# Optimization experiments

Hardware: AMD Instinct MI355X
Metric: run time of the kernel (lower is better)

## Reference

```python
import jax, jax.numpy as jnp
import numpy as np

NUM_EMBEDDINGS = 2048
EMBEDDING_DIM = 256
COMMITMENT_COST = 0.25


def setup_inputs() -> dict:
    key = jax.random.key(0)
    k1, k2 = jax.random.split(key)
    inputs = jax.random.normal(k1, (2, EMBEDDING_DIM, 24, 24, 24), dtype=jnp.float32)
    embedding_weight = jax.random.normal(k2, (NUM_EMBEDDINGS, EMBEDDING_DIM), dtype=jnp.float32)
    return {"inputs": inputs, "embedding_weight": embedding_weight}


def reference(inputs, embedding_weight):
    # [B, C, D, H, W] -> [B, D, H, W, C]
    x = jnp.transpose(inputs, (0, 2, 3, 4, 1))
    in_shape = x.shape
    flat = x.reshape(-1, EMBEDDING_DIM)  # [N, D]

    distances = (
        jnp.sum(flat * flat, axis=1, keepdims=True)
        + jnp.sum(embedding_weight * embedding_weight, axis=1)
        - 2.0 * flat @ embedding_weight.T
    )
    encoding_indices = jnp.argmin(distances, axis=1)  # [N]
    encodings = jax.nn.one_hot(encoding_indices, NUM_EMBEDDINGS, dtype=jnp.float32)  # [N, K]

    # Gather instead of one_hot @ W (same math, no redundant GEMM)
    quantized = embedding_weight[encoding_indices].reshape(in_shape)

    e_latent_loss = jnp.mean((jax.lax.stop_gradient(quantized) - x) ** 2)
    loss = COMMITMENT_COST * e_latent_loss

    # Straight-through estimator
    quantized_st = x + jax.lax.stop_gradient(quantized - x)

    avg_probs = jnp.mean(encodings, axis=0)
    perplexity = jnp.exp(-jnp.sum(avg_probs * jnp.log(avg_probs + 1e-10)))

    quantized_out = jnp.transpose(quantized_st, (0, 4, 1, 2, 3))
    return (loss, quantized_out, perplexity, encodings, encoding_indices[:, None])
```

## Files before the change

### kernel.cpp

```cpp
#include <hip/hip_runtime.h>

#define S_SP   13824
#define CHAN   256
#define NQ     27648
#define KCODES 2048
#define CS     3538944
#define OFF_Q   1
#define OFF_PPL 7077889
#define OFF_ENC 7077890LL
#define OFF_IDX 63700994LL

typedef __bf16 bf16x8 __attribute__((ext_vector_type(8)));
typedef float  f32x4  __attribute__((ext_vector_type(4)));

#define GLOAD_LDS16(g, s)                                                      \
  __builtin_amdgcn_global_load_lds(                                            \
      (const __attribute__((address_space(1))) void*)(g),                      \
      (__attribute__((address_space(3))) void*)(s), 16, 0, 0)

__device__ __forceinline__ unsigned int f2bf(float f) {
  unsigned int u = __float_as_uint(f);
  unsigned int r = u + 0x7FFFu + ((u >> 16) & 1u);
  return r >> 16;
}
__device__ __forceinline__ float bf2f(unsigned int h) {
  return __uint_as_float(h << 16);
}
__device__ __forceinline__ void fsplit(float f, unsigned int& hi, unsigned int& lo) {
  hi = f2bf(f);
  float r = f - bf2f(hi);
  lo = f2bf(r);
}

__global__ __launch_bounds__(256) void prep_wx(const float* __restrict__ W,
                                               const float* __restrict__ X,
                                               unsigned short* __restrict__ Wh,
                                               unsigned short* __restrict__ Wl,
                                               float* __restrict__ wn,
                                               unsigned short* __restrict__ Xh,
                                               unsigned short* __restrict__ Xl,
                                               float* __restrict__ xn,
                                               int* __restrict__ zero_base) {
  __shared__ float xs[32 * 257];
  int t = threadIdx.x;
  if (blockIdx.x < 256) {
    if (blockIdx.x == 0) {
      for (int j = t; j < 2050; j += 256) zero_base[j] = 0;
    }
    int g = blockIdx.x * 256 + t;
    int row = g >> 5;
    int d0 = (g & 31) * 8;
    const float* Wp = W + (size_t)row * CHAN + d0;
    float v[8];
    *(float4*)(v) = *(const float4*)Wp;
    *(float4*)(v + 4) = *(const float4*)(Wp + 4);
    float s = 0.f;
    unsigned int h[8], l[8];
#pragma unroll
    for (int j = 0; j < 8; ++j) {
      s = fmaf(v[j], v[j], s);
      fsplit(v[j], h[j], l[j]);
    }
    int4 ph, pl;
    ph.x = (int)(h[0] | (h[1] << 16)); ph.y = (int)(h[2] | (h[3] << 16));
    ph.z = (int)(h[4] | (h[5] << 16)); ph.w = (int)(h[6] | (h[7] << 16));
    pl.x = (int)(l[0] | (l[1] << 16)); pl.y = (int)(l[2] | (l[3] << 16));
    pl.z = (int)(l[4] | (l[5] << 16)); pl.w = (int)(l[6] | (l[7] << 16));
    *(int4*)(Wh + (size_t)row * CHAN + d0) = ph;
    *(int4*)(Wl + (size_t)row * CHAN + d0) = pl;
    for (int off = 16; off; off >>= 1) s += __shfl_down(s, off);
    if ((t & 31) == 0) wn[row] = s;
    return;
  }
  int qb = (blockIdx.x - 256) * 32;
  int b = qb / S_SP, s0 = qb % S_SP;
  const float* xp = X + (size_t)b * CS + s0;
  int q = t & 31;
  int db = t >> 5;
  for (int r = 0; r < 32; ++r) {
    int d = db + (r << 3);
    xs[q * 257 + d] = xp[(size_t)d * S_SP + q];
  }
  __syncthreads();
  int row = t >> 3, c8 = t & 7;
  size_t obase = (size_t)(qb + row) * CHAN;
  const float* rp0 = xs + row * 257;
  float ss = 0.f;
#pragma unroll
  for (int j = 0; j < 4; ++j) {
    int d = j * 64 + c8 * 8;
    const float* rp = rp0 + d;
    unsigned int h[8], l[8];
#pragma unroll
    for (int e = 0; e < 8; ++e) {
      float v = rp[e];
      ss = fmaf(v, v, ss);
      fsplit(v, h[e], l[e]);
    }
    int4 ph, pl;
    ph.x = (int)(h[0] | (h[1] << 16)); ph.y = (int)(h[2] | (h[3] << 16));
    ph.z = (int)(h[4] | (h[5] << 16)); ph.w = (int)(h[6] | (h[7] << 16));
    pl.x = (int)(l[0] | (l[1] << 16)); pl.y = (int)(l[2] | (l[3] << 16));
    pl.z = (int)(l[4] | (l[5] << 16)); pl.w = (int)(l[6] | (l[7] << 16));
    *(int4*)(Xh + obase + d) = ph;
    *(int4*)(Xl + obase + d) = pl;
  }
  ss += __shfl_xor(ss, 1);
  ss += __shfl_xor(ss, 2);
  ss += __shfl_xor(ss, 4);
  if (c8 == 0) xn[qb + row] = ss;
}

__global__ __launch_bounds__(256, 2) void dist_mfma(const unsigned short* __restrict__ Xh,
                                                    const unsigned short* __restrict__ Xl,
                                                    const unsigned short* __restrict__ Wh,
                                                    const unsigned short* __restrict__ Wl,
                                                    const float* __restrict__ wn,
                                                    float* __restrict__ rB1,
                                                    int* __restrict__ rI1,
                                                    float* __restrict__ rB2) {
  __shared__ __align__(16) unsigned short sW[2][2][4096];
  __shared__ float wnl[1024];
  int t = threadIdx.x;
  int w = t >> 6, l = t & 63;
  int lr = l & 15, lc = l >> 4;
  int kg = blockIdx.x & 1;
  int qb = (blockIdx.x >> 1) * 128;
  int kofs = kg << 10;

  for (int j = t; j < 1024; j += 256) wnl[j] = wn[kofs + j];

  bf16x8 ah[2][8], al[2][8];
#pragma unroll
  for (int s = 0; s < 2; ++s) {
    size_t base = (size_t)(qb + w * 32 + s * 16 + lr) * CHAN + lc * 8;
#pragma unroll
    for (int c = 0; c < 8; ++c) {
      ah[s][c] = *(const bf16x8*)(Xh + base + c * 32);
      al[s][c] = *(const bf16x8*)(Xl + base + c * 32);
    }
  }

  float b1[2][4], b2[2][4]; int i1[2][4];
#pragma unroll
  for (int s = 0; s < 2; ++s)
#pragma unroll
    for (int r = 0; r < 4; ++r) { b1[s][r] = 3.4e38f; b2[s][r] = 3.4e38f; i1[s][r] = 0; }

  auto stage = [&](int buf, int kt) {
    size_t rb = (size_t)(kofs + (kt << 4) + lr) * CHAN + lc * 8;
    GLOAD_LDS16(Wh + rb + w * 32,        &sW[buf][0][w * 512]);
    GLOAD_LDS16(Wh + rb + (w + 4) * 32,  &sW[buf][0][(w + 4) * 512]);
    GLOAD_LDS16(Wl + rb + w * 32,        &sW[buf][1][w * 512]);
    GLOAD_LDS16(Wl + rb + (w + 4) * 32,  &sW[buf][1][(w + 4) * 512]);
  };

  stage(0, 0);
  __syncthreads();

  for (int kt = 0; kt < 64; ++kt) {
    int cur = kt & 1;
    if (kt < 63) stage(cur ^ 1, kt + 1);
    f32x4 a0 = {0.f, 0.f, 0.f, 0.f}, a1 = {0.f, 0.f, 0.f, 0.f};
#pragma unroll
    for (int c = 0; c < 8; ++c) {
      bf16x8 bh = *(const bf16x8*)&sW[cur][0][c * 512 + (l << 3)];
      bf16x8 bl = *(const bf16x8*)&sW[cur][1][c * 512 + (l << 3)];
      a0 = __builtin_amdgcn_mfma_f32_16x16x32_bf16(ah[0][c], bh, a0, 0, 0, 0);
      a1 = __builtin_amdgcn_mfma_f32_16x16x32_bf16(ah[1][c], bh, a1, 0, 0, 0);
      a0 = __builtin_amdgcn_mfma_f32_16x16x32_bf16(al[0][c], bh, a0, 0, 0, 0);
      a1 = __builtin_amdgcn_mfma_f32_16x16x32_bf16(al[1][c], bh, a1, 0, 0, 0);
      a0 = __builtin_amdgcn_mfma_f32_16x16x32_bf16(ah[0][c], bl, a0, 0, 0, 0);
      a1 = __builtin_amdgcn_mfma_f32_16x16x32_bf16(ah[1][c], bl, a1, 0, 0, 0);
    }
    int k = kofs + (kt << 4) + lr;
    float wnk = wnl[(kt << 4) + lr];
#pragma unroll
    for (int r = 0; r < 4; ++r) {
      float s0 = fmaf(-2.0f, a0[r], wnk);
      bool lt0 = s0 < b1[0][r];
      b2[0][r] = fminf(b2[0][r], fmaxf(s0, b1[0][r]));
      b1[0][r] = lt0 ? s0 : b1[0][r];
      i1[0][r] = lt0 ? k : i1[0][r];
      float s1 = fmaf(-2.0f, a1[r], wnk);
      bool lt1 = s1 < b1[1][r];
      b2[1][r] = fminf(b2[1][r], fmaxf(s1, b1[1][r]));
      b1[1][r] = lt1 ? s1 : b1[1][r];
      i1[1][r] = lt1 ? k : i1[1][r];
    }
    __syncthreads();
  }

#pragma unroll
  for (int m = 1; m < 16; m <<= 1) {
#pragma unroll
    for (int s = 0; s < 2; ++s)
#pragma unroll
      for (int r = 0; r < 4; ++r) {
        float ob1 = __shfl_xor(b1[s][r], m);
        int   oi  = __shfl_xor(i1[s][r], m);
        float ob2 = __shfl_xor(b2[s][r], m);
        bool sw = (ob1 < b1[s][r]) || (ob1 == b1[s][r] && oi < i1[s][r]);
        b2[s][r] = fminf(fmaxf(b1[s][r], ob1), fminf(b2[s][r], ob2));
        b1[s][r] = sw ? ob1 : b1[s][r];
        i1[s][r] = sw ? oi : i1[s][r];
      }
  }
  if (lr == 0) {
#pragma unroll
    for (int s = 0; s < 2; ++s)
#pragma unroll
      for (int r = 0; r < 4; ++r) {
        int q = qb + w * 32 + s * 16 + lc * 4 + r;
        size_t o = (size_t)kg * NQ + q;
        rB1[o] = b1[s][r]; rI1[o] = i1[s][r]; rB2[o] = b2[s][r];
      }
  }
}

__global__ __launch_bounds__(256) void merge_k(const float* __restrict__ rB1,
                                               const int* __restrict__ rI1,
                                               const float* __restrict__ rB2,
                                               const float* __restrict__ xn,
                                               float* __restrict__ idx_out,
                                               int* __restrict__ flagcount,
                                               int2* __restrict__ flaglist,
                                               int* __restrict__ counts,
                                               float* __restrict__ loss_acc) {
  __shared__ float wred[4];
  int t = threadIdx.x;
  int n = blockIdx.x * 256 + t;
  float B1 = rB1[n]; int I1 = rI1[n]; float B2 = rB2[n];
  float c1 = rB1[NQ + n]; int ci = rI1[NQ + n]; float c2 = rB2[NQ + n];
  bool sw = (c1 < B1) || (c1 == B1 && ci < I1);
  float nb2 = fminf(fmaxf(B1, c1), fminf(B2, c2));
  float nb1 = sw ? c1 : B1;
  int   ni  = sw ? ci : I1;
  if (nb2 - nb1 < 0.05f) {
    int slot = atomicAdd(flagcount, 1);
    flaglist[slot] = make_int2(n, ni);
  }
  idx_out[n] = (float)ni;
  atomicAdd(&counts[ni], 1);

  float lq = xn[n] + nb1;
  for (int off = 32; off; off >>= 1) lq += __shfl_down(lq, off);
  if ((t & 63) == 0) wred[t >> 6] = lq;
  __syncthreads();
  if (t == 0) atomicAdd(loss_acc, wred[0] + wred[1] + wred[2] + wred[3]);
}

__global__ __launch_bounds__(256) void refine2(const float* __restrict__ X,
                                               const float* __restrict__ W,
                                               const int* __restrict__ flagcount,
                                               const int2* __restrict__ flaglist,
                                               float* __restrict__ idx_out,
                                               int* __restrict__ counts) {
  __shared__ double xd[CHAN];
  __shared__ double rv[256];
  __shared__ int    ri[256];
  int t = threadIdx.x;
  int cnt = flagcount[0];
  for (int jj = blockIdx.x; jj < cnt; jj += gridDim.x) {
    __syncthreads();
    int2 e = flaglist[jj];
    int n = e.x, prov = e.y;
    int b = n / S_SP, s = n % S_SP;
    xd[t] = (double)X[(size_t)b * CS + (size_t)t * S_SP + s];
    __syncthreads();

    double best = 1e300;
    int bi = 1 << 30;
    for (int j8 = 0; j8 < 8; ++j8) {
      int k = t * 8 + j8;
      const float* Wp = W + (size_t)k * CHAN;
      double dsum = 0.0;
      for (int d = 0; d < CHAN; ++d) {
        double df = xd[d] - (double)Wp[d];
        dsum = fma(df, df, dsum);
      }
      if (dsum < best) { best = dsum; bi = k; }
    }
    rv[t] = best; ri[t] = bi;
    __syncthreads();
    for (int off = 128; off > 0; off >>= 1) {
      if (t < off) {
        if (rv[t + off] < rv[t] || (rv[t + off] == rv[t] && ri[t + off] < ri[t])) {
          rv[t] = rv[t + off]; ri[t] = ri[t + off];
        }
      }
      __syncthreads();
    }
    if (t == 0) {
      int fin = ri[0];
      idx_out[n] = (float)fin;
      if (fin != prov) {
        atomicAdd(&counts[prov], -1);
        atomicAdd(&counts[fin], 1);
      }
    }
  }
}

__global__ __launch_bounds__(256) void emit_q(const float* __restrict__ W,
                                              float* __restrict__ outF) {
  __shared__ int sidx[64];
  int t = threadIdx.x;
  int qb = blockIdx.x * 64;
  if (t < 64) sidx[t] = (int)outF[OFF_IDX + qb + t];
  __syncthreads();

  {
    f32x4 z = {0.f, 0.f, 0.f, 0.f};
    float* rp = outF + OFF_ENC + (size_t)qb * KCODES + t * 4;
#pragma unroll 4
    for (int q = 0; q < 64; ++q) {
      *(f32x4*)rp = z;
      *(f32x4*)(rp + 1024) = z;
      rp += KCODES;
    }
  }
  __syncthreads();
  if (t < 64) outF[OFF_ENC + (size_t)(qb + t) * KCODES + sidx[t]] = 1.0f;

  int q = t & 63, cg = t >> 6;
  int n = qb + q;
  int idx = sidx[q];
  int b = n / S_SP, s = n % S_SP;
  const float* Wp = W + (size_t)idx * CHAN;
  float* qp = outF + OFF_Q + (size_t)b * CS + s;
#pragma unroll 8
  for (int k = 0; k < 64; ++k) {
    int c = cg + (k << 2);
    qp[(size_t)c * S_SP] = Wp[c];
  }
}

__global__ __launch_bounds__(256) void finalize(const int* __restrict__ counts,
                                                const float* __restrict__ loss_acc,
                                                float* __restrict__ outF) {
  __shared__ double red[256];
  int t = threadIdx.x;
  double H = 0.0;
  for (int k = t; k < KCODES; k += 256) {
    double p = (double)counts[k] / (double)NQ;
    H += p * log(p + 1e-10);
  }
  red[t] = H;
  __syncthreads();
  for (int off = 128; off > 0; off >>= 1) {
    if (t < off) red[t] += red[t + off];
    __syncthreads();
  }
  if (t == 0) {
    outF[0] = 0.25f * (loss_acc[0] / 7077888.0f);
    outF[OFF_PPL] = (float)exp(-red[0]);
  }
}

extern "C" void kernel_launch(void* const* d_in, const int* in_sizes, int n_in,
                              void* d_out, int out_size, void* d_ws, size_t ws_size,
                              hipStream_t stream) {
  const float* X = (const float*)d_in[0];
  const float* W = (const float*)d_in[1];
  float* outF = (float*)d_out;
  char* ws = (char*)d_ws;
  float* wn        = (float*)ws;
  int*   counts    = (int*)(ws + 8192);
  float* loss_acc  = (float*)(ws + 16384);
  int*   flagcount = (int*)(ws + 16388);
  int2*  flaglist  = (int2*)(ws + 32768);
  float* rB1       = (float*)(ws + 262144);
  int*   rI1       = (int*)(ws + 483328);
  float* rB2       = (float*)(ws + 704512);
  float* xn        = (float*)(ws + 925696);
  unsigned short* Wh = (unsigned short*)(ws + 1048576);
  unsigned short* Wl = (unsigned short*)(ws + 2097152);
  unsigned short* Xh = (unsigned short*)(ws + 3145728);
  unsigned short* Xl = Xh + (size_t)NQ * CHAN;

  prep_wx<<<256 + NQ / 32, 256, 0, stream>>>(W, X, Wh, Wl, wn, Xh, Xl, xn,
                                             (int*)(ws + 8192));
  dist_mfma<<<(NQ / 128) * 2, 256, 0, stream>>>(Xh, Xl, Wh, Wl, wn, rB1, rI1, rB2);
  merge_k<<<NQ / 256, 256, 0, stream>>>(rB1, rI1, rB2, xn, outF + OFF_IDX,
                                        flagcount, flaglist, counts, loss_acc);
  refine2<<<256, 256, 0, stream>>>(X, W, flagcount, flaglist, outF + OFF_IDX, counts);
  emit_q<<<NQ / 64, 256, 0, stream>>>(W, outF);
  finalize<<<1, 256, 0, stream>>>(counts, loss_acc, outF);
}
```

Measured before the change: 261.5 us.

## Stream codebook tiles into registers directly, dropping LDS staging and barriers

```diff
diff --git a/kernel.cpp b/kernel.cpp
--- a/kernel.cpp
+++ b/kernel.cpp
@@ -12,11 +12,6 @@
 
 typedef __bf16 bf16x8 __attribute__((ext_vector_type(8)));
 typedef float  f32x4  __attribute__((ext_vector_type(4)));
-
-#define GLOAD_LDS16(g, s)                                                      \
-  __builtin_amdgcn_global_load_lds(                                            \
-      (const __attribute__((address_space(1))) void*)(g),                      \
-      (__attribute__((address_space(3))) void*)(s), 16, 0, 0)
 
 __device__ __forceinline__ unsigned int f2bf(float f) {
   unsigned int u = __float_as_uint(f);
@@ -119,7 +114,6 @@
                                                     float* __restrict__ rB1,
                                                     int* __restrict__ rI1,
                                                     float* __restrict__ rB2) {
-  __shared__ __align__(16) unsigned short sW[2][2][4096];
   __shared__ float wnl[1024];
   int t = threadIdx.x;
   int w = t >> 6, l = t & 63;
@@ -147,34 +141,7 @@
 #pragma unroll
     for (int r = 0; r < 4; ++r) { b1[s][r] = 3.4e38f; b2[s][r] = 3.4e38f; i1[s][r] = 0; }
 
-  auto stage = [&](int buf, int kt) {
-    size_t rb = (size_t)(kofs + (kt << 4) + lr) * CHAN + lc * 8;
-    GLOAD_LDS16(Wh + rb + w * 32,        &sW[buf][0][w * 512]);
-    GLOAD_LDS16(Wh + rb + (w + 4) * 32,  &sW[buf][0][(w + 4) * 512]);
-    GLOAD_LDS16(Wl + rb + w * 32,        &sW[buf][1][w * 512]);
-    GLOAD_LDS16(Wl + rb + (w + 4) * 32,  &sW[buf][1][(w + 4) * 512]);
-  };
-
-  stage(0, 0);
-  __syncthreads();
-
-  for (int kt = 0; kt < 64; ++kt) {
-    int cur = kt & 1;
-    if (kt < 63) stage(cur ^ 1, kt + 1);
-    f32x4 a0 = {0.f, 0.f, 0.f, 0.f}, a1 = {0.f, 0.f, 0.f, 0.f};
-#pragma unroll
-    for (int c = 0; c < 8; ++c) {
-      bf16x8 bh = *(const bf16x8*)&sW[cur][0][c * 512 + (l << 3)];
-      bf16x8 bl = *(const bf16x8*)&sW[cur][1][c * 512 + (l << 3)];
-      a0 = __builtin_amdgcn_mfma_f32_16x16x32_bf16(ah[0][c], bh, a0, 0, 0, 0);
-      a1 = __builtin_amdgcn_mfma_f32_16x16x32_bf16(ah[1][c], bh, a1, 0, 0, 0);
-      a0 = __builtin_amdgcn_mfma_f32_16x16x32_bf16(al[0][c], bh, a0, 0, 0, 0);
-      a1 = __builtin_amdgcn_mfma_f32_16x16x32_bf16(al[1][c], bh, a1, 0, 0, 0);
-      a0 = __builtin_amdgcn_mfma_f32_16x16x32_bf16(ah[0][c], bl, a0, 0, 0, 0);
-      a1 = __builtin_amdgcn_mfma_f32_16x16x32_bf16(ah[1][c], bl, a1, 0, 0, 0);
-    }
-    int k = kofs + (kt << 4) + lr;
-    float wnk = wnl[(kt << 4) + lr];
+  auto select = [&](const f32x4& a0, const f32x4& a1, int k, float wnk) {
 #pragma unroll
     for (int r = 0; r < 4; ++r) {
       float s0 = fmaf(-2.0f, a0[r], wnk);
@@ -188,8 +155,51 @@
       b1[1][r] = lt1 ? s1 : b1[1][r];
       i1[1][r] = lt1 ? k : i1[1][r];
     }
-    __syncthreads();
-  }
+  };
+
+  __syncthreads();
+
+  const unsigned short* ph  = Wh + (size_t)(kofs + lr) * CHAN + lc * 8;
+  const unsigned short* pl_ = Wl + (size_t)(kofs + lr) * CHAN + lc * 8;
+
+  bf16x8 bh[4], bl[4];
+#pragma unroll
+  for (int c = 0; c < 4; ++c) {
+    bh[c] = *(const bf16x8*)(ph + c * 32);
+    bl[c] = *(const bf16x8*)(pl_ + c * 32);
+  }
+
+  f32x4 pa0, pa1;
+  int   pk = 0;
+  float pwnk = 0.f;
+
+  for (int kt = 0; kt < 64; ++kt) {
+    f32x4 a0 = {0.f, 0.f, 0.f, 0.f}, a1 = {0.f, 0.f, 0.f, 0.f};
+#pragma unroll
+    for (int c = 0; c < 8; ++c) {
+      const int sl = c & 3;
+      a0 = __builtin_amdgcn_mfma_f32_16x16x32_bf16(ah[0][c], bh[sl], a0, 0, 0, 0);
+      a1 = __builtin_amdgcn_mfma_f32_16x16x32_bf16(ah[1][c], bh[sl], a1, 0, 0, 0);
+      a0 = __builtin_amdgcn_mfma_f32_16x16x32_bf16(al[0][c], bh[sl], a0, 0, 0, 0);
+      a1 = __builtin_amdgcn_mfma_f32_16x16x32_bf16(al[1][c], bh[sl], a1, 0, 0, 0);
+      a0 = __builtin_amdgcn_mfma_f32_16x16x32_bf16(ah[0][c], bl[sl], a0, 0, 0, 0);
+      a1 = __builtin_amdgcn_mfma_f32_16x16x32_bf16(ah[1][c], bl[sl], a1, 0, 0, 0);
+      if (c < 4) {
+        bh[sl] = *(const bf16x8*)(ph + (c + 4) * 32);
+        bl[sl] = *(const bf16x8*)(pl_ + (c + 4) * 32);
+      } else {
+        bh[sl] = *(const bf16x8*)(ph + 16 * CHAN + (c - 4) * 32);
+        bl[sl] = *(const bf16x8*)(pl_ + 16 * CHAN + (c - 4) * 32);
+      }
+    }
+    if (kt) select(pa0, pa1, pk, pwnk);
+    pa0 = a0; pa1 = a1;
+    pk = kofs + (kt << 4) + lr;
+    pwnk = wnl[(kt << 4) + lr];
+    ph  += 16 * CHAN;
+    pl_ += 16 * CHAN;
+  }
+  select(pa0, pa1, pk, pwnk);
 
 #pragma unroll
   for (int m = 1; m < 16; m <<= 1) {
```

After: 398.2 us. +52.3%, slower.

## Switch distance GEMM to 32x32x16 MFMA with software-pipelined argmin selection

Applied to the files above, without the earlier changes.

```diff
diff --git a/kernel.cpp b/kernel.cpp
--- a/kernel.cpp
+++ b/kernel.cpp
@@ -12,6 +12,7 @@
 
 typedef __bf16 bf16x8 __attribute__((ext_vector_type(8)));
 typedef float  f32x4  __attribute__((ext_vector_type(4)));
+typedef float  f32x16 __attribute__((ext_vector_type(16)));
 
 #define GLOAD_LDS16(g, s)                                                      \
   __builtin_amdgcn_global_load_lds(                                            \
@@ -119,102 +120,110 @@
                                                     float* __restrict__ rB1,
                                                     int* __restrict__ rI1,
                                                     float* __restrict__ rB2) {
-  __shared__ __align__(16) unsigned short sW[2][2][4096];
+  __shared__ __align__(16) unsigned short sW[2][2][8192];
   __shared__ float wnl[1024];
   int t = threadIdx.x;
   int w = t >> 6, l = t & 63;
-  int lr = l & 15, lc = l >> 4;
+  int lcol = l & 31;
+  int lkg  = l >> 5;
   int kg = blockIdx.x & 1;
   int qb = (blockIdx.x >> 1) * 128;
   int kofs = kg << 10;
 
   for (int j = t; j < 1024; j += 256) wnl[j] = wn[kofs + j];
 
-  bf16x8 ah[2][8], al[2][8];
-#pragma unroll
-  for (int s = 0; s < 2; ++s) {
-    size_t base = (size_t)(qb + w * 32 + s * 16 + lr) * CHAN + lc * 8;
-#pragma unroll
-    for (int c = 0; c < 8; ++c) {
-      ah[s][c] = *(const bf16x8*)(Xh + base + c * 32);
-      al[s][c] = *(const bf16x8*)(Xl + base + c * 32);
-    }
-  }
-
-  float b1[2][4], b2[2][4]; int i1[2][4];
-#pragma unroll
-  for (int s = 0; s < 2; ++s)
-#pragma unroll
-    for (int r = 0; r < 4; ++r) { b1[s][r] = 3.4e38f; b2[s][r] = 3.4e38f; i1[s][r] = 0; }
+  bf16x8 ah[16], al[16];
+  {
+    size_t base = (size_t)(qb + w * 32 + lcol) * CHAN + (lkg << 3);
+#pragma unroll
+    for (int kc = 0; kc < 16; ++kc) {
+      ah[kc] = *(const bf16x8*)(Xh + base + kc * 16);
+      al[kc] = *(const bf16x8*)(Xl + base + kc * 16);
+    }
+  }
+
+  float b1[16], b2[16]; int i1[16];
+#pragma unroll
+  for (int r = 0; r < 16; ++r) { b1[r] = 3.4e38f; b2[r] = 3.4e38f; i1[r] = 0; }
 
   auto stage = [&](int buf, int kt) {
-    size_t rb = (size_t)(kofs + (kt << 4) + lr) * CHAN + lc * 8;
-    GLOAD_LDS16(Wh + rb + w * 32,        &sW[buf][0][w * 512]);
-    GLOAD_LDS16(Wh + rb + (w + 4) * 32,  &sW[buf][0][(w + 4) * 512]);
-    GLOAD_LDS16(Wl + rb + w * 32,        &sW[buf][1][w * 512]);
-    GLOAD_LDS16(Wl + rb + (w + 4) * 32,  &sW[buf][1][(w + 4) * 512]);
+    size_t rb = (size_t)(kofs + (kt << 5) + lcol) * CHAN + (lkg << 3);
+#pragma unroll
+    for (int j = 0; j < 4; ++j) {
+      int kc = 4 * w + j;
+      GLOAD_LDS16(Wh + rb + kc * 16, &sW[buf][0][kc * 512]);
+      GLOAD_LDS16(Wl + rb + kc * 16, &sW[buf][1][kc * 512]);
+    }
   };
 
+  auto compute = [&](int cur, f32x16& out) {
+    f32x16 a = {0.f,0.f,0.f,0.f,0.f,0.f,0.f,0.f,0.f,0.f,0.f,0.f,0.f,0.f,0.f,0.f};
+#pragma unroll
+    for (int kc = 0; kc < 16; ++kc) {
+      bf16x8 bh = *(const bf16x8*)&sW[cur][0][kc * 512 + l * 8];
+      bf16x8 bl = *(const bf16x8*)&sW[cur][1][kc * 512 + l * 8];
+      a = __builtin_amdgcn_mfma_f32_32x32x16_bf16(ah[kc], bh, a, 0, 0, 0);
+      a = __builtin_amdgcn_mfma_f32_32x32x16_bf16(al[kc], bh, a, 0, 0, 0);
+      a = __builtin_amdgcn_mfma_f32_32x32x16_bf16(ah[kc], bl, a, 0, 0, 0);
+    }
+    out = a;
+  };
+
+  auto select = [&](const f32x16& a, int k, float wnk) {
+#pragma unroll
+    for (int r = 0; r < 16; ++r) {
+      float s = fmaf(-2.0f, a[r], wnk);
+      bool lt = s < b1[r];
+      b2[r] = fminf(b2[r], fmaxf(s, b1[r]));
+      b1[r] = lt ? s : b1[r];
+      i1[r] = lt ? k : i1[r];
+    }
+  };
+
   stage(0, 0);
   __syncthreads();
 
-  for (int kt = 0; kt < 64; ++kt) {
+  f32x16 pa;
+  int   pk   = kofs + lcol;
+  float pwnk = wnl[lcol];
+  stage(1, 1);
+  compute(0, pa);
+  __syncthreads();
+
+  for (int kt = 1; kt < 32; ++kt) {
     int cur = kt & 1;
-    if (kt < 63) stage(cur ^ 1, kt + 1);
-    f32x4 a0 = {0.f, 0.f, 0.f, 0.f}, a1 = {0.f, 0.f, 0.f, 0.f};
-#pragma unroll
-    for (int c = 0; c < 8; ++c) {
-      bf16x8 bh = *(const bf16x8*)&sW[cur][0][c * 512 + (l << 3)];
-      bf16x8 bl = *(const bf16x8*)&sW[cur][1][c * 512 + (l << 3)];
-      a0 = __builtin_amdgcn_mfma_f32_16x16x32_bf16(ah[0][c], bh, a0, 0, 0, 0);
-      a1 = __builtin_amdgcn_mfma_f32_16x16x32_bf16(ah[1][c], bh, a1, 0, 0, 0);
-      a0 = __builtin_amdgcn_mfma_f32_16x16x32_bf16(al[0][c], bh, a0, 0, 0, 0);
-      a1 = __builtin_amdgcn_mfma_f32_16x16x32_bf16(al[1][c], bh, a1, 0, 0, 0);
-      a0 = __builtin_amdgcn_mfma_f32_16x16x32_bf16(ah[0][c], bl, a0, 0, 0, 0);
-      a1 = __builtin_amdgcn_mfma_f32_16x16x32_bf16(ah[1][c], bl, a1, 0, 0, 0);
-    }
-    int k = kofs + (kt << 4) + lr;
-    float wnk = wnl[(kt << 4) + lr];
-#pragma unroll
-    for (int r = 0; r < 4; ++r) {
-      float s0 = fmaf(-2.0f, a0[r], wnk);
-      bool lt0 = s0 < b1[0][r];
-      b2[0][r] = fminf(b2[0][r], fmaxf(s0, b1[0][r]));
-      b1[0][r] = lt0 ? s0 : b1[0][r];
-      i1[0][r] = lt0 ? k : i1[0][r];
-      float s1 = fmaf(-2.0f, a1[r], wnk);
-      bool lt1 = s1 < b1[1][r];
-      b2[1][r] = fminf(b2[1][r], fmaxf(s1, b1[1][r]));
-      b1[1][r] = lt1 ? s1 : b1[1][r];
-      i1[1][r] = lt1 ? k : i1[1][r];
-    }
-    __syncthreads();
-  }
-
-#pragma unroll
-  for (int m = 1; m < 16; m <<= 1) {
-#pragma unroll
-    for (int s = 0; s < 2; ++s)
-#pragma unroll
-      for (int r = 0; r < 4; ++r) {
-        float ob1 = __shfl_xor(b1[s][r], m);
-        int   oi  = __shfl_xor(i1[s][r], m);
-        float ob2 = __shfl_xor(b2[s][r], m);
-        bool sw = (ob1 < b1[s][r]) || (ob1 == b1[s][r] && oi < i1[s][r]);
-        b2[s][r] = fminf(fmaxf(b1[s][r], ob1), fminf(b2[s][r], ob2));
-        b1[s][r] = sw ? ob1 : b1[s][r];
-        i1[s][r] = sw ? oi : i1[s][r];
-      }
-  }
-  if (lr == 0) {
-#pragma unroll
-    for (int s = 0; s < 2; ++s)
-#pragma unroll
-      for (int r = 0; r < 4; ++r) {
-        int q = qb + w * 32 + s * 16 + lc * 4 + r;
-        size_t o = (size_t)kg * NQ + q;
-        rB1[o] = b1[s][r]; rI1[o] = i1[s][r]; rB2[o] = b2[s][r];
-      }
+    if (kt < 31) stage(cur ^ 1, kt + 1);
+    f32x16 a;
+    compute(cur, a);
+    select(pa, pk, pwnk);
+    pa = a;
+    pk = kofs + (kt << 5) + lcol;
+    pwnk = wnl[(kt << 5) + lcol];
+    __syncthreads();
+  }
+  select(pa, pk, pwnk);
+
+#pragma unroll
+  for (int m = 1; m < 32; m <<= 1) {
+#pragma unroll
+    for (int r = 0; r < 16; ++r) {
+      float ob1 = __shfl_xor(b1[r], m);
+      int   oi  = __shfl_xor(i1[r], m);
+      float ob2 = __shfl_xor(b2[r], m);
+      bool sw = (ob1 < b1[r]) || (ob1 == b1[r] && oi < i1[r]);
+      b2[r] = fminf(fmaxf(b1[r], ob1), fminf(b2[r], ob2));
+      b1[r] = sw ? ob1 : b1[r];
+      i1[r] = sw ? oi : i1[r];
+    }
+  }
+  if (lcol == 0) {
+#pragma unroll
+    for (int r = 0; r < 16; ++r) {
+      int row = (r & 3) + 8 * (r >> 2) + 4 * lkg;
+      int q = qb + w * 32 + row;
+      size_t o = (size_t)kg * NQ + q;
+      rB1[o] = b1[r]; rI1[o] = i1[r]; rB2[o] = b2[r];
+    }
   }
 }
 
```

New measurement: 254.2 us. -2.8%, faster.
